# Optimization experiments

Hardware: AMD Instinct MI355X
Metric: run time of the kernel (lower is better)

Reference implementation:

```python
import jax, jax.numpy as jnp
import numpy as np

H = 256
NUM_REL = 480
NUM_ENT = 23000
N_TRIPLES = 8192
T = 10  # cur_ts == path_len window


def _lin_params(key, din, dout):
    kw, _ = jax.random.split(key)
    W = jax.random.normal(kw, (din, dout), dtype=jnp.float32) * 0.02
    b = jnp.zeros((dout,), dtype=jnp.float32)
    return W, b


def setup_inputs() -> dict:
    key = jax.random.key(0)
    ks = jax.random.split(key, 16)
    pre_emb = jax.random.normal(ks[0], (NUM_ENT, H), dtype=jnp.float32)
    r_emb = jax.random.normal(ks[1], (NUM_REL, H), dtype=jnp.float32)
    # history counts: sparse non-negative (zeros are masked to -1e9 in softmax)
    part = jax.random.uniform(ks[2], (N_TRIPLES, T * NUM_REL), dtype=jnp.float32)
    mask = jax.random.uniform(ks[3], (N_TRIPLES, T * NUM_REL)) < 0.3
    partial_embeding = jnp.where(mask, part, 0.0)
    sub_idx = jax.random.randint(ks[4], (N_TRIPLES,), 0, NUM_ENT)
    rel_idx = jax.random.randint(ks[5], (N_TRIPLES,), 0, NUM_REL)
    obj_idx = jax.random.randint(ks[6], (N_TRIPLES,), 0, NUM_ENT)
    Wm1, bm1 = _lin_params(ks[7], H, 2 * H)
    Wm2, bm2 = _lin_params(ks[8], 2 * H, H)
    Wattn, battn = _lin_params(ks[9], H, H)
    Wh1, bh1 = _lin_params(ks[10], H, H)
    Wh2, bh2 = _lin_params(ks[11], H, H)
    Walign, balign = _lin_params(ks[12], H, H)
    Wih = jax.random.normal(ks[13], (H, 3 * H), dtype=jnp.float32) * 0.02
    Whh = jax.random.normal(ks[14], (H, 3 * H), dtype=jnp.float32) * 0.02
    bih = jnp.zeros((3 * H,), dtype=jnp.float32)
    bhh = jnp.zeros((3 * H,), dtype=jnp.float32)
    return dict(pre_emb=pre_emb, r_emb=r_emb, partial_embeding=partial_embeding,
                sub_idx=sub_idx, rel_idx=rel_idx, obj_idx=obj_idx, cur_ts=T,
                Wm1=Wm1, bm1=bm1, Wm2=Wm2, bm2=bm2, Wattn=Wattn, battn=battn,
                Wh1=Wh1, bh1=bh1, Wh2=Wh2, bh2=bh2, Walign=Walign, balign=balign,
                Wih=Wih, Whh=Whh, bih=bih, bhh=bhh)


def _gru_cell(x, h, Wih, Whh, bih, bhh):
    # torch.nn.GRUCell math
    gi = x @ Wih + bih
    gh = h @ Whh + bhh
    i_r, i_z, i_n = jnp.split(gi, 3, axis=-1)
    h_r, h_z, h_n = jnp.split(gh, 3, axis=-1)
    r = jax.nn.sigmoid(i_r + h_r)
    z = jax.nn.sigmoid(i_z + h_z)
    n = jnp.tanh(i_n + r * h_n)
    return (1.0 - z) * n + z * h


def reference(pre_emb, r_emb, partial_embeding, sub_idx, rel_idx, obj_idx, cur_ts,
              Wm1, bm1, Wm2, bm2, Wattn, battn, Wh1, bh1, Wh2, bh2,
              Walign, balign, Wih, Whh, bih, bhh):
    n = partial_embeding.shape[0]
    num_rel = r_emb.shape[0]
    t = cur_ts  # path window covers [0, cur_ts)
    # relation mapping
    mapped_rel = (r_emb @ Wm1 + bm1) @ Wm2 + bm2            # [R, H]
    q_rel = mapped_rel[rel_idx]                               # [N, H]
    # attention logits base (loop-invariant): q W_attn mapped_rel^T
    base = (q_rel @ Wattn + battn) @ mapped_rel.T            # [N, R]
    # [N, t*R] -> [t, N, R] time-major slices
    hist = partial_embeding[:, : t * num_rel].reshape(n, t, num_rel).swapaxes(0, 1)
    h0 = jnp.zeros((n, mapped_rel.shape[1]), dtype=pre_emb.dtype)

    def step(h, cur):
        attn = cur * base
        attn = jax.nn.softmax(jnp.where(attn == 0, -1e9, attn), axis=1)
        x = attn @ mapped_rel                                 # [N, H]
        return _gru_cell(x, h, Wih, Whh, bih, bhh), None

    gru_hidden, _ = jax.lax.scan(step, h0, hist)
    # predicted history + match loss
    predicted_hist = 0.1 * ((q_rel @ Wh1 + bh1) @ Wh2 + bh2) + q_rel
    match_loss = jnp.mean((predicted_hist - gru_hidden) ** 2)
    # forward_forth (distmult)
    h2 = _gru_cell(q_rel, predicted_hist, Wih, Whh, bih, bhh)  # [N, H]
    sub = pre_emb[sub_idx]
    score_ = ((sub @ Walign + balign) * h2) @ (pre_emb @ Walign + balign).T  # [N, E]
    # BCE(sigmoid(score_), one_hot(obj)): per-elem -y*logsig(s) - (1-y)*logsig(-s)
    pos = score_[jnp.arange(n), obj_idx]
    path_loss = (-jnp.sum(jax.nn.log_sigmoid(-score_)) - jnp.sum(pos)) / (score_.size)
    score = jax.nn.sigmoid(score_)
    return match_loss, path_loss, score
```

## Files before the change

kernel.cpp:

```cpp
#include <hip/hip_runtime.h>
#include <hip/hip_bf16.h>
#include <stdint.h>

#define DEV __device__ __forceinline__

typedef unsigned short u16;
typedef __attribute__((ext_vector_type(8))) short bf16x8;
typedef __attribute__((ext_vector_type(4))) float f32x4;
typedef __attribute__((ext_vector_type(4))) unsigned short u16x4;

constexpr int H  = 256;
constexpr int R  = 480;
constexpr int NE = 23000;
constexpr int NT = 8192;
constexpr int TT = 10;

DEV u16 f2b(float f) {
  union { float f; unsigned u; } x; x.f = f;
  unsigned u = x.u;
  return (u16)((u + 0x7fffu + ((u >> 16) & 1u)) >> 16);
}
DEV float b2f(u16 h) {
  union { unsigned u; float f; } x; x.u = ((unsigned)h) << 16;
  return x.f;
}

DEV void gload_lds16(const u16* g, u16* lds) {
  __builtin_amdgcn_global_load_lds(
      (const __attribute__((address_space(1))) unsigned int*)g,
      (__attribute__((address_space(3))) unsigned int*)lds, 16, 0, 0);
}

__global__ void init_k(float* __restrict__ h, unsigned int* __restrict__ hb) {
  const int idx = blockIdx.x * 256 + threadIdx.x;
  h[idx] = 0.f;
  if (idx < (NT * H) / 2) hb[idx] = 0u;
}

__launch_bounds__(256)
__global__ void stageA_k(const float* __restrict__ r_emb,
                         const float* __restrict__ Wm1, const float* __restrict__ bm1,
                         const float* __restrict__ Wm2, const float* __restrict__ bm2,
                         const float* __restrict__ Wattn, const float* __restrict__ battn,
                         const float* __restrict__ Wih,
                         const float* __restrict__ Wh1, const float* __restrict__ bh1,
                         const float* __restrict__ Wh2, const float* __restrict__ bh2,
                         const float* __restrict__ Whh, const float* __restrict__ bhh,
                         const float* __restrict__ bih,
                         float* __restrict__ mapped, float* __restrict__ t1,
                         float* __restrict__ Pg, float* __restrict__ G2,
                         u16* __restrict__ MWT) {
  __shared__ float re[256], hid[512], mp[256], p1l[256], Pl[256];
  const int r = blockIdx.x, j = threadIdx.x;
  re[j] = r_emb[(size_t)r * 256 + j];
  __syncthreads();
  float s0 = bm1[j], s1 = bm1[j + 256];
  for (int k = 0; k < 256; ++k) {
    const float a = re[k];
    s0 += a * Wm1[(size_t)k * 512 + j];
    s1 += a * Wm1[(size_t)k * 512 + j + 256];
  }
  hid[j] = s0; hid[j + 256] = s1;
  __syncthreads();
  float m = bm2[j];
  for (int k = 0; k < 512; ++k) m += hid[k] * Wm2[(size_t)k * 256 + j];
  mp[j] = m; mapped[(size_t)r * 256 + j] = m;
  __syncthreads();
  float tv = battn[j];
  for (int k = 0; k < 256; ++k) tv += mp[k] * Wattn[(size_t)k * 256 + j];
  t1[(size_t)r * 256 + j] = tv;
  float mw0 = 0.f, mw1 = 0.f, mw2 = 0.f;
  for (int k = 0; k < 256; ++k) {
    const float a = mp[k];
    mw0 += a * Wih[(size_t)k * 768 + j];
    mw1 += a * Wih[(size_t)k * 768 + j + 256];
    mw2 += a * Wih[(size_t)k * 768 + j + 512];
  }
  MWT[(size_t)j * 480 + r] = f2b(mw0);
  MWT[(size_t)(j + 256) * 480 + r] = f2b(mw1);
  MWT[(size_t)(j + 512) * 480 + r] = f2b(mw2);
  float pv = bh1[j];
  for (int k = 0; k < 256; ++k) pv += mp[k] * Wh1[(size_t)k * 256 + j];
  p1l[j] = pv;
  __syncthreads();
  float Pv = bh2[j];
  for (int k = 0; k < 256; ++k) Pv += p1l[k] * Wh2[(size_t)k * 256 + j];
  Pv = 0.1f * Pv + mp[j];
  Pl[j] = Pv; Pg[(size_t)r * 256 + j] = Pv;
  __syncthreads();
  float pw0 = bhh[j], pw1 = bhh[j + 256], pw2 = bhh[j + 512];
  for (int k = 0; k < 256; ++k) {
    const float a = Pl[k];
    pw0 += a * Whh[(size_t)k * 768 + j];
    pw1 += a * Whh[(size_t)k * 768 + j + 256];
    pw2 += a * Whh[(size_t)k * 768 + j + 512];
  }
  const float rg = 1.f / (1.f + __expf(-(mw0 + bih[j] + pw0)));
  const float zg = 1.f / (1.f + __expf(-(mw1 + bih[j + 256] + pw1)));
  const float ng = tanhf(mw2 + bih[j + 512] + rg * pw2);
  G2[(size_t)r * 256 + j] = (1.f - zg) * ng + zg * Pv;
}

__global__ void sgemm_bt_k(const float* __restrict__ A, const float* __restrict__ W,
                           float* __restrict__ C, int M, int N, int K) {
  const int idx = blockIdx.x * 256 + threadIdx.x;
  if (idx >= M * N) return;
  const int i = idx / N, j = idx % N;
  float s = 0.f;
  const float* a = A + (size_t)i * K;
  const float* w = W + (size_t)j * K;
  for (int k = 0; k < K; ++k) s += a[k] * w[k];
  C[idx] = s;
}

__global__ void prep_k(const float* __restrict__ Whh, const float* __restrict__ Walign,
                       const float* __restrict__ bih, const float* __restrict__ bhh,
                       u16* __restrict__ WhhT, u16* __restrict__ WalignT,
                       float* __restrict__ bsum) {
  const int b = blockIdx.x, tid = threadIdx.x;
  if (b < 768) {
    WhhT[(size_t)b * 256 + tid] = f2b(Whh[(size_t)tid * 768 + b]);
  } else if (b < 1024) {
    const int n = b - 768;
    WalignT[(size_t)n * 256 + tid] = f2b(Walign[(size_t)tid * 256 + n]);
  } else {
    const int c = (b - 1024) * 256 + tid;
    if (c < 768) bsum[c] = bih[c] + (c < 512 ? bhh[c] : 0.f);
  }
}

__global__ void softmax_all_k(const float* __restrict__ part, const float* __restrict__ B480,
                              const int* __restrict__ rel_idx, u16* __restrict__ attn,
                              int t0) {
  const int task = blockIdx.x * 4 + (threadIdx.x >> 6);
  const int lane = threadIdx.x & 63;
  const int tt = task >> 13;
  const int i  = task & (NT - 1);
  const float* cur = part + (size_t)i * (TT * R) + (size_t)(t0 + tt) * R;
  const float* b = B480 + (size_t)rel_idx[i] * R;
  float v[8];
  float m = -3e38f;
  #pragma unroll
  for (int j = 0; j < 8; ++j) {
    const int r = lane + j * 64;
    float val = -1e9f;
    if (r < R) {
      const float c = cur[r];
      val = (c == 0.f) ? -1e9f : c * b[r];
      m = fmaxf(m, val);
    }
    v[j] = val;
  }
  #pragma unroll
  for (int o = 32; o; o >>= 1) m = fmaxf(m, __shfl_xor(m, o));
  float s = 0.f;
  #pragma unroll
  for (int j = 0; j < 8; ++j) {
    const int r = lane + j * 64;
    if (r < R) { v[j] = __expf(v[j] - m); s += v[j]; }
  }
  #pragma unroll
  for (int o = 32; o; o >>= 1) s += __shfl_xor(s, o);
  const float inv = 1.f / s;
  u16* arow = attn + (size_t)task * R;
  #pragma unroll
  for (int j = 0; j < 8; ++j) {
    const int r = lane + j * 64;
    if (r < R) arow[r] = f2b(v[j] * inv);
  }
}

__launch_bounds__(256)
__global__ void ghgates_k(const u16* __restrict__ hb, const u16* __restrict__ WhhT,
                          const float* __restrict__ bhh, const u16* __restrict__ gi,
                          float* __restrict__ h, u16* __restrict__ hb_out) {
  __shared__ __align__(16) u16 As[64 * 32];
  __shared__ __align__(16) u16 Bs[192 * 32];
  const int tid = threadIdx.x;
  const int lane = tid & 63;
  const int wv = tid >> 6;
  const int cg = blockIdx.x;
  const int m0 = blockIdx.y * 64;
  const int wr0 = wv * 16;
  const int fr = lane & 15;
  const int fq = lane >> 4;

  const int row_e = m0 + wr0 + fr;
  u16x4 g_r[4], g_z[4], g_n[4];
  f32x4 hv[4], bn;
  #pragma unroll
  for (int nc = 0; nc < 4; ++nc) {
    const int c = cg * 64 + nc * 16 + fq * 4;
    const size_t gb = (size_t)row_e * 768 + c;
    g_r[nc] = *(const u16x4*)&gi[gb];
    g_z[nc] = *(const u16x4*)&gi[gb + 256];
    g_n[nc] = *(const u16x4*)&gi[gb + 512];
    hv[nc] = *(const f32x4*)&h[(size_t)row_e * H + c];
  }
  {
    const int c = cg * 64 + fq * 4;
    bn = *(const f32x4*)&bhh[512 + c];
  }

  f32x4 acc[12] = {};
  for (int k0 = 0; k0 < H; k0 += 32) {
    __syncthreads();
    {
      const int row = tid >> 2, cc = tid & 3;
      gload_lds16(hb + (size_t)(m0 + row) * H + k0 + cc * 8,
                  &As[(wv * 64) * 8]);
    }
    #pragma unroll
    for (int it = 0; it < 3; ++it) {
      const int c = it * 256 + tid;
      const int vrow = c >> 2, cc = c & 3;
      const int col = (vrow >> 6) * 256 + cg * 64 + (vrow & 63);
      gload_lds16(WhhT + (size_t)col * H + k0 + cc * 8,
                  &Bs[(it * 256 + wv * 64) * 8]);
    }
    __syncthreads();
    const bf16x8 a = *(const bf16x8*)&As[(wr0 + fr) * 32 + fq * 8];
    bf16x8 b[12];
    #pragma unroll
    for (int ni = 0; ni < 12; ++ni)
      b[ni] = *(const bf16x8*)&Bs[(ni * 16 + fr) * 32 + fq * 8];
    #pragma unroll
    for (int ni = 0; ni < 12; ++ni)
      acc[ni] = __builtin_amdgcn_mfma_f32_16x16x32_bf16(b[ni], a, acc[ni], 0, 0, 0);
  }

  #pragma unroll
  for (int nc = 0; nc < 4; ++nc) {
    const int c = cg * 64 + nc * 16 + fq * 4;
    const f32x4 bnn = *(const f32x4*)&bhh[512 + c];
    const size_t hi = (size_t)row_e * H + c;
    f32x4 hn;
    u16x4 hb4;
    #pragma unroll
    for (int j = 0; j < 4; ++j) {
      const float rg = 1.f / (1.f + __expf(-(b2f(g_r[nc][j]) + acc[nc][j])));
      const float zg = 1.f / (1.f + __expf(-(b2f(g_z[nc][j]) + acc[4 + nc][j])));
      const float ng = tanhf(b2f(g_n[nc][j]) + rg * (acc[8 + nc][j] + bnn[j]));
      hn[j] = (1.f - zg) * ng + zg * hv[nc][j];
      hb4[j] = f2b(hn[j]);
    }
    *(f32x4*)&h[hi] = hn;
    *(u16x4*)&hb_out[hi] = hb4;
  }
}

__global__ void gather_sub_k(const float* __restrict__ pre, const int* __restrict__ sub,
                             u16* __restrict__ sb) {
  const int q = blockIdx.x * 256 + threadIdx.x;
  const int i = q >> 6, c = (q & 63) * 4;
  const f32x4 v = *(const f32x4*)&pre[(size_t)sub[i] * H + c];
  u16x4 o;
  #pragma unroll
  for (int j = 0; j < 4; ++j) o[j] = f2b(v[j]);
  *(u16x4*)&sb[(size_t)q * 4] = o;
}
__global__ void cvt_pre_k(const float* __restrict__ pre, u16* __restrict__ pb) {
  const int q = blockIdx.x * 256 + threadIdx.x;
  const f32x4 v = *(const f32x4*)&pre[(size_t)q * 4];
  u16x4 o;
  #pragma unroll
  for (int j = 0; j < 4; ++j) o[j] = f2b(v[j]);
  *(u16x4*)&pb[(size_t)q * 4] = o;
}

__global__ void pos_k(const u16* __restrict__ lhs, const u16* __restrict__ alT,
                      const int* __restrict__ obj, float* __restrict__ pos) {
  const int row = blockIdx.x * 4 + (threadIdx.x >> 6);
  const int lane = threadIdx.x & 63;
  const u16x4 av = *(const u16x4*)&lhs[(size_t)row * H + lane * 4];
  const u16x4 bv = *(const u16x4*)&alT[(size_t)obj[row] * H + lane * 4];
  float s = 0.f;
  #pragma unroll
  for (int j = 0; j < 4; ++j) s += b2f(av[j]) * b2f(bv[j]);
  #pragma unroll
  for (int o = 32; o; o >>= 1) s += __shfl_down(s, o);
  if (lane == 0) pos[row] = s;
}

__global__ void finalize_k(const float* __restrict__ mp, const float* __restrict__ sp,
                           const float* __restrict__ pos, float* __restrict__ out) {
  const int tid = threadIdx.x;
  float s1 = 0.f, s2 = 0.f, s3 = 0.f;
  for (int i = tid; i < 128; i += 256) s1 += mp[i];
  for (int i = tid; i < 11520; i += 256) s2 += sp[i];
  for (int i = tid; i < 8192; i += 256) s3 += pos[i];
  #pragma unroll
  for (int o = 32; o; o >>= 1) {
    s1 += __shfl_down(s1, o); s2 += __shfl_down(s2, o); s3 += __shfl_down(s3, o);
  }
  __shared__ float r1[4], r2[4], r3[4];
  if ((tid & 63) == 0) { r1[tid >> 6] = s1; r2[tid >> 6] = s2; r3[tid >> 6] = s3; }
  __syncthreads();
  if (tid == 0) {
    const float a = r1[0] + r1[1] + r1[2] + r1[3];
    const float b = r2[0] + r2[1] + r2[2] + r2[3];
    const float c = r3[0] + r3[1] + r3[2] + r3[3];
    out[0] = a / 2097152.f;
    out[1] = (b - c) / 188416000.f;
  }
}

template <int MODE>
__launch_bounds__(256)
__global__ void gemm_k(const u16* __restrict__ A, const u16* __restrict__ Bt,
                       const float* __restrict__ bias,
                       float* __restrict__ Cf, u16* __restrict__ Cb,
                       int M, int N, int K,
                       float* __restrict__ out2, float* __restrict__ part,
                       const int* __restrict__ rel_idx, const float* __restrict__ Pf,
                       const float* __restrict__ G2f, const float* __restrict__ hf) {
  __shared__ __align__(16) u16 As[128 * 32];
  __shared__ __align__(16) u16 Bs[128 * 32];
  __shared__ float red[4];
  const int tid = threadIdx.x;
  const int lane = tid & 63;
  const int wv = tid >> 6;
  const int nbx = gridDim.x;
  int flat = blockIdx.y * nbx + blockIdx.x;
  const int nwg = nbx * gridDim.y;
  if ((nwg & 7) == 0) flat = (flat & 7) * (nwg >> 3) + (flat >> 3);
  const int bx = flat % nbx;
  const int by = flat / nbx;
  const int m0 = by * 128;
  const int n0 = bx * 128;
  const int wm = (wv >> 1) * 64;
  const int wn = (wv & 1) * 64;
  const int fr = lane & 15;
  const int fq = lane >> 4;
  f32x4 acc[4][4] = {};

  for (int k0 = 0; k0 < K; k0 += 32) {
    __syncthreads();
    #pragma unroll
    for (int it = 0; it < 2; ++it) {
      const int c = it * 256 + tid;
      const int row = c >> 2;
      const int cc = c & 3;
      int gr = m0 + row; gr = gr < M ? gr : M - 1;
      gload_lds16(A + (size_t)gr * K + k0 + cc * 8, &As[(it * 256 + wv * 64) * 8]);
      int nr = n0 + row; nr = nr < N ? nr : N - 1;
      gload_lds16(Bt + (size_t)nr * K + k0 + cc * 8, &Bs[(it * 256 + wv * 64) * 8]);
    }
    __syncthreads();
    bf16x8 a[4], b[4];
    #pragma unroll
    for (int mi = 0; mi < 4; ++mi)
      a[mi] = *(const bf16x8*)&As[(wm + mi * 16 + fr) * 32 + fq * 8];
    #pragma unroll
    for (int ni = 0; ni < 4; ++ni)
      b[ni] = *(const bf16x8*)&Bs[(wn + ni * 16 + fr) * 32 + fq * 8];
    #pragma unroll
    for (int mi = 0; mi < 4; ++mi)
      #pragma unroll
      for (int ni = 0; ni < 4; ++ni)
        acc[mi][ni] = __builtin_amdgcn_mfma_f32_16x16x32_bf16(b[ni], a[mi], acc[mi][ni], 0, 0, 0);
  }

  float local = 0.f;
  #pragma unroll
  for (int mi = 0; mi < 4; ++mi) {
    const int rowm = m0 + wm + mi * 16 + fr;
    int rel = 0;
    if (MODE == 2) rel = rel_idx[rowm];
    #pragma unroll
    for (int ni = 0; ni < 4; ++ni) {
      const int col = n0 + wn + ni * 16 + fq * 4;
      if (rowm < M && col < N) {
        f32x4 v = acc[mi][ni];
        if (MODE == 0) {
          if (bias != nullptr) {
            const f32x4 bv = *(const f32x4*)&bias[col];
            #pragma unroll
            for (int j = 0; j < 4; ++j) v[j] += bv[j];
          }
          if (Cf) *(f32x4*)&Cf[(size_t)rowm * N + col] = v;
          if (Cb) {
            u16x4 o;
            #pragma unroll
            for (int j = 0; j < 4; ++j) o[j] = f2b(v[j]);
            *(u16x4*)&Cb[(size_t)rowm * N + col] = o;
          }
        } else if (MODE == 1) {
          f32x4 sg;
          #pragma unroll
          for (int j = 0; j < 4; ++j) {
            const float s = v[j];
            const float sig = 1.f / (1.f + __expf(-s));
            sg[j] = sig;
            const float om = 1.f - sig;
            local += (om > 0.f) ? -__logf(om) : s;
          }
          *(f32x4*)&out2[(size_t)rowm * N + col] = sg;
        } else {
          const f32x4 bv = *(const f32x4*)&bias[col];
          const f32x4 Pv = *(const f32x4*)&Pf[(size_t)rel * H + col];
          const f32x4 Gv = *(const f32x4*)&G2f[(size_t)rel * H + col];
          const f32x4 hv = *(const f32x4*)&hf[(size_t)rowm * H + col];
          u16x4 o;
          #pragma unroll
          for (int j = 0; j < 4; ++j) {
            const float d = Pv[j] - hv[j];
            local += d * d;
            o[j] = f2b((v[j] + bv[j]) * Gv[j]);
          }
          *(u16x4*)&Cb[(size_t)rowm * N + col] = o;
        }
      }
    }
  }
  if (MODE != 0) {
    #pragma unroll
    for (int o = 32; o; o >>= 1) local += __shfl_down(local, o);
    if (lane == 0) red[wv] = local;
    __syncthreads();
    if (tid == 0) part[blockIdx.y * gridDim.x + blockIdx.x] = red[0] + red[1] + red[2] + red[3];
  }
}

extern "C" void kernel_launch(void* const* d_in, const int* in_sizes, int n_in,
                              void* d_out, int out_size, void* d_ws, size_t ws_size,
                              hipStream_t stream) {
  const float* pre_emb = (const float*)d_in[0];
  const float* r_emb   = (const float*)d_in[1];
  const float* part_e  = (const float*)d_in[2];
  const int*   sub_idx = (const int*)d_in[3];
  const int*   rel_idx = (const int*)d_in[4];
  const int*   obj_idx = (const int*)d_in[5];
  const float* Wm1 = (const float*)d_in[7];  const float* bm1 = (const float*)d_in[8];
  const float* Wm2 = (const float*)d_in[9];  const float* bm2 = (const float*)d_in[10];
  const float* Wattn = (const float*)d_in[11]; const float* battn = (const float*)d_in[12];
  const float* Wh1 = (const float*)d_in[13]; const float* bh1 = (const float*)d_in[14];
  const float* Wh2 = (const float*)d_in[15]; const float* bh2 = (const float*)d_in[16];
  const float* Walign = (const float*)d_in[17]; const float* balign = (const float*)d_in[18];
  const float* Wih = (const float*)d_in[19]; const float* Whh = (const float*)d_in[20];
  const float* bih = (const float*)d_in[21]; const float* bhh = (const float*)d_in[22];
  float* out = (float*)d_out;

  char* w = (char*)d_ws;
  size_t off = 0;
  auto alloc = [&](size_t bytes) -> void* {
    off = (off + 255) & ~(size_t)255;
    void* p = w + off;
    off += bytes;
    return p;
  };
  float* mapped = (float*)alloc((size_t)R * H * 4);
  float* t1     = (float*)alloc((size_t)R * H * 4);
  float* B480   = (float*)alloc((size_t)R * R * 4);
  float* P      = (float*)alloc((size_t)R * H * 4);
  float* G2     = (float*)alloc((size_t)R * H * 4);
  u16* MWT      = (u16*)alloc((size_t)768 * R * 2);
  u16* WhhT     = (u16*)alloc((size_t)768 * H * 2);
  u16* WalignT  = (u16*)alloc((size_t)H * H * 2);
  float* bsum   = (float*)alloc(768 * 4);
  float* hbuf   = (float*)alloc((size_t)NT * H * 4);
  u16* hb0      = (u16*)alloc((size_t)NT * H * 2);
  u16* hb1      = (u16*)alloc((size_t)NT * H * 2);
  u16* lhs_b    = (u16*)alloc((size_t)NT * H * 2);
  u16* sub_b    = (u16*)alloc((size_t)NT * H * 2);
  u16* pre_b    = (u16*)alloc((size_t)NE * H * 2);
  u16* alT      = (u16*)alloc((size_t)NE * H * 2);
  float* mpart  = (float*)alloc(128 * 4);
  float* spart  = (float*)alloc(11520 * 4);
  float* posar  = (float*)alloc(8192 * 4);
  const size_t fixed_end = off;

  int chunkT = TT;
  u16 *attn_all = nullptr, *gi_all = nullptr;
  for (;;) {
    off = fixed_end;
    attn_all = (u16*)alloc((size_t)chunkT * NT * R * 2);
    gi_all   = (u16*)alloc((size_t)chunkT * NT * 768 * 2);
    if (off <= ws_size) break;
    if (chunkT == 1) return;
    chunkT = 1;
  }

  init_k<<<NT, 256, 0, stream>>>(hbuf, (unsigned int*)hb0);

  stageA_k<<<R, 256, 0, stream>>>(r_emb, Wm1, bm1, Wm2, bm2, Wattn, battn, Wih,
                                  Wh1, bh1, Wh2, bh2, Whh, bhh, bih,
                                  mapped, t1, P, G2, MWT);
  sgemm_bt_k<<<(R * R + 255) / 256, 256, 0, stream>>>(t1, mapped, B480, R, R, H);
  prep_k<<<1027, 256, 0, stream>>>(Whh, Walign, bih, bhh, WhhT, WalignT, bsum);

  u16* hcur = hb0;
  u16* hnxt = hb1;
  for (int t0 = 0; t0 < TT; t0 += chunkT) {
    softmax_all_k<<<chunkT * (NT / 4), 256, 0, stream>>>(part_e, B480, rel_idx, attn_all, t0);
    gemm_k<0><<<dim3(6, chunkT * (NT / 128)), 256, 0, stream>>>(
        attn_all, MWT, bsum, nullptr, gi_all, chunkT * NT, 768, R,
        nullptr, nullptr, nullptr, nullptr, nullptr, nullptr);
    for (int tt = 0; tt < chunkT; ++tt) {
      ghgates_k<<<dim3(4, NT / 64), 256, 0, stream>>>(
          hcur, WhhT, bhh, gi_all + (size_t)tt * NT * 768, hbuf, hnxt);
      u16* tmp = hcur; hcur = hnxt; hnxt = tmp;
    }
  }

  gather_sub_k<<<NT / 4, 256, 0, stream>>>(pre_emb, sub_idx, sub_b);
  gemm_k<2><<<dim3(2, 64), 256, 0, stream>>>(
      sub_b, WalignT, balign, nullptr, lhs_b, NT, H, H,
      nullptr, mpart, rel_idx, P, G2, hbuf);

  cvt_pre_k<<<NE / 4, 256, 0, stream>>>(pre_emb, pre_b);
  gemm_k<0><<<dim3(2, 180), 256, 0, stream>>>(
      pre_b, WalignT, balign, nullptr, alT, NE, H, H,
      nullptr, nullptr, nullptr, nullptr, nullptr, nullptr);

  gemm_k<1><<<dim3(180, 64), 256, 0, stream>>>(
      lhs_b, alT, nullptr, nullptr, nullptr, NT, NE, H,
      out + 2, spart, nullptr, nullptr, nullptr, nullptr);

  pos_k<<<2048, 256, 0, stream>>>(lhs_b, alT, obj_idx, posar);
  finalize_k<<<1, 256, 0, stream>>>(mpart, spart, posar, out);
}
```

Measured before the change: 1.134 ms.

## Fuse GRU time loop into one persistent scan kernel with LDS-resident hidden state

Replaces the ten per-timestep ghgates launches with a single scan kernel. Each block owns 32 rows and keeps the hidden state in registers, with a bf16 copy in swizzled LDS, across all timesteps, while double-buffering the Whh tiles. This removes the per-step launch overhead and the global round-trips of h. The generic GEMM moves to a K=64 step with an XOR-swizzled LDS layout, and the attention and MWT buffers are padded from 480 to 512 columns so K is aligned. The cost is only 256 blocks for the scan, which limits occupancy, plus Whh being re-streamed for every block and every step.

```diff
diff --git a/kernel.cpp b/kernel.cpp
--- a/kernel.cpp
+++ b/kernel.cpp
@@ -11,6 +11,7 @@
 
 constexpr int H  = 256;
 constexpr int R  = 480;
+constexpr int RP = 512;
 constexpr int NE = 23000;
 constexpr int NT = 8192;
 constexpr int TT = 10;
@@ -29,12 +30,6 @@
   __builtin_amdgcn_global_load_lds(
       (const __attribute__((address_space(1))) unsigned int*)g,
       (__attribute__((address_space(3))) unsigned int*)lds, 16, 0, 0);
-}
-
-__global__ void init_k(float* __restrict__ h, unsigned int* __restrict__ hb) {
-  const int idx = blockIdx.x * 256 + threadIdx.x;
-  h[idx] = 0.f;
-  if (idx < (NT * H) / 2) hb[idx] = 0u;
 }
 
 __launch_bounds__(256)
@@ -76,9 +71,9 @@
     mw1 += a * Wih[(size_t)k * 768 + j + 256];
     mw2 += a * Wih[(size_t)k * 768 + j + 512];
   }
-  MWT[(size_t)j * 480 + r] = f2b(mw0);
-  MWT[(size_t)(j + 256) * 480 + r] = f2b(mw1);
-  MWT[(size_t)(j + 512) * 480 + r] = f2b(mw2);
+  MWT[(size_t)j * RP + r] = f2b(mw0);
+  MWT[(size_t)(j + 256) * RP + r] = f2b(mw1);
+  MWT[(size_t)(j + 512) * RP + r] = f2b(mw2);
   float pv = bh1[j];
   for (int k = 0; k < 256; ++k) pv += mp[k] * Wh1[(size_t)k * 256 + j];
   p1l[j] = pv;
@@ -130,13 +125,12 @@
 }
 
 __global__ void softmax_all_k(const float* __restrict__ part, const float* __restrict__ B480,
-                              const int* __restrict__ rel_idx, u16* __restrict__ attn,
-                              int t0) {
+                              const int* __restrict__ rel_idx, u16* __restrict__ attn) {
   const int task = blockIdx.x * 4 + (threadIdx.x >> 6);
   const int lane = threadIdx.x & 63;
   const int tt = task >> 13;
   const int i  = task & (NT - 1);
-  const float* cur = part + (size_t)i * (TT * R) + (size_t)(t0 + tt) * R;
+  const float* cur = part + (size_t)i * (TT * R) + (size_t)tt * R;
   const float* b = B480 + (size_t)rel_idx[i] * R;
   float v[8];
   float m = -3e38f;
@@ -162,90 +156,124 @@
   #pragma unroll
   for (int o = 32; o; o >>= 1) s += __shfl_xor(s, o);
   const float inv = 1.f / s;
-  u16* arow = attn + (size_t)task * R;
+  u16* arow = attn + (size_t)task * RP;
   #pragma unroll
   for (int j = 0; j < 8; ++j) {
     const int r = lane + j * 64;
-    if (r < R) arow[r] = f2b(v[j] * inv);
+    arow[r] = (r < R) ? f2b(v[j] * inv) : (u16)0;
   }
 }
 
 __launch_bounds__(256)
-__global__ void ghgates_k(const u16* __restrict__ hb, const u16* __restrict__ WhhT,
-                          const float* __restrict__ bhh, const u16* __restrict__ gi,
-                          float* __restrict__ h, u16* __restrict__ hb_out) {
-  __shared__ __align__(16) u16 As[64 * 32];
-  __shared__ __align__(16) u16 Bs[192 * 32];
+__global__ void scan_k(const u16* __restrict__ WhhT, const float* __restrict__ bhh,
+                       const u16* __restrict__ gi_all, float* __restrict__ hbuf) {
+  __shared__ __align__(16) u16 As[32 * 256];
+  __shared__ __align__(16) u16 Bs[2][192 * 64];
   const int tid = threadIdx.x;
   const int lane = tid & 63;
   const int wv = tid >> 6;
-  const int cg = blockIdx.x;
-  const int m0 = blockIdx.y * 64;
-  const int wr0 = wv * 16;
+  const int rf = wv >> 1;
+  const int ch = wv & 1;
   const int fr = lane & 15;
   const int fq = lane >> 4;
-
-  const int row_e = m0 + wr0 + fr;
-  u16x4 g_r[4], g_z[4], g_n[4];
-  f32x4 hv[4], bn;
-  #pragma unroll
-  for (int nc = 0; nc < 4; ++nc) {
-    const int c = cg * 64 + nc * 16 + fq * 4;
-    const size_t gb = (size_t)row_e * 768 + c;
-    g_r[nc] = *(const u16x4*)&gi[gb];
-    g_z[nc] = *(const u16x4*)&gi[gb + 256];
-    g_n[nc] = *(const u16x4*)&gi[gb + 512];
-    hv[nc] = *(const f32x4*)&h[(size_t)row_e * H + c];
-  }
-  {
-    const int c = cg * 64 + fq * 4;
-    bn = *(const f32x4*)&bhh[512 + c];
-  }
-
-  f32x4 acc[12] = {};
-  for (int k0 = 0; k0 < H; k0 += 32) {
+  const int row_l = rf * 16 + fr;
+  const int grow = blockIdx.x * 32 + row_l;
+  const int sw = (fr & 7) * 8;
+
+  auto stageB = [&](int buf, int cg, int k0) {
+    #pragma unroll
+    for (int it = 0; it < 6; ++it) {
+      const int c = it * 256 + tid;
+      const int vr = c >> 3, s = c & 7;
+      const int vcol = ((vr >> 6) * 256) + cg * 64 + (vr & 63);
+      gload_lds16(WhhT + (size_t)vcol * 256 + k0 + ((s ^ (vr & 7)) * 8),
+                  &Bs[buf][(it * 256 + wv * 64) * 8]);
+    }
+  };
+
+  float hreg[4][2][4];
+  #pragma unroll
+  for (int cg = 0; cg < 4; ++cg)
+    #pragma unroll
+    for (int nn = 0; nn < 2; ++nn)
+      #pragma unroll
+      for (int j = 0; j < 4; ++j) hreg[cg][nn][j] = 0.f;
+
+  for (int t = 0; t < TT; ++t) {
+    const u16* gi = gi_all + (size_t)t * NT * 768;
+    #pragma unroll
+    for (int cg = 0; cg < 4; ++cg) {
+      f32x4 acc[6] = {};
+      u16x4 gv[3][2];
+      #pragma unroll
+      for (int nn = 0; nn < 2; ++nn) {
+        const int c = cg * 64 + ch * 32 + nn * 16 + fq * 4;
+        const size_t gb = (size_t)grow * 768 + c;
+        gv[0][nn] = *(const u16x4*)&gi[gb];
+        gv[1][nn] = *(const u16x4*)&gi[gb + 256];
+        gv[2][nn] = *(const u16x4*)&gi[gb + 512];
+      }
+      if (t > 0) {
+        stageB(0, cg, 0);
+        #pragma unroll
+        for (int ki = 0; ki < 4; ++ki) {
+          const int cb = ki & 1;
+          if (ki < 3) {
+            stageB(cb ^ 1, cg, (ki + 1) * 64);
+            asm volatile("s_waitcnt vmcnt(6)" ::: "memory");
+          } else {
+            asm volatile("s_waitcnt vmcnt(0)" ::: "memory");
+          }
+          __builtin_amdgcn_sched_barrier(0);
+          __builtin_amdgcn_s_barrier();
+          #pragma unroll
+          for (int kk = 0; kk < 2; ++kk) {
+            const int ko = (ki * 64 + kk * 32 + fq * 8) ^ sw;
+            const bf16x8 a = *(const bf16x8*)&As[row_l * 256 + ko];
+            const int bo = (kk * 32 + fq * 8) ^ sw;
+            #pragma unroll
+            for (int g = 0; g < 3; ++g)
+              #pragma unroll
+              for (int nn = 0; nn < 2; ++nn) {
+                const int vr = g * 64 + ch * 32 + nn * 16 + fr;
+                const bf16x8 b = *(const bf16x8*)&Bs[cb][vr * 64 + bo];
+                acc[g * 2 + nn] =
+                    __builtin_amdgcn_mfma_f32_16x16x32_bf16(b, a, acc[g * 2 + nn], 0, 0, 0);
+              }
+          }
+          __builtin_amdgcn_s_barrier();
+        }
+      }
+      #pragma unroll
+      for (int nn = 0; nn < 2; ++nn) {
+        const int c = cg * 64 + ch * 32 + nn * 16 + fq * 4;
+        const f32x4 bn = *(const f32x4*)&bhh[512 + c];
+        #pragma unroll
+        for (int j = 0; j < 4; ++j) {
+          const float rg = 1.f / (1.f + __expf(-(b2f(gv[0][nn][j]) + acc[nn][j])));
+          const float zg = 1.f / (1.f + __expf(-(b2f(gv[1][nn][j]) + acc[2 + nn][j])));
+          const float ng = tanhf(b2f(gv[2][nn][j]) + rg * (acc[4 + nn][j] + bn[j]));
+          hreg[cg][nn][j] = (1.f - zg) * ng + zg * hreg[cg][nn][j];
+        }
+      }
+    }
+    #pragma unroll
+    for (int cg = 0; cg < 4; ++cg)
+      #pragma unroll
+      for (int nn = 0; nn < 2; ++nn) {
+        const int c = cg * 64 + ch * 32 + nn * 16 + fq * 4;
+        u16x4 o;
+        #pragma unroll
+        for (int j = 0; j < 4; ++j) o[j] = f2b(hreg[cg][nn][j]);
+        *(u16x4*)&As[row_l * 256 + (c ^ sw)] = o;
+        if (t == TT - 1) {
+          f32x4 hv;
+          #pragma unroll
+          for (int j = 0; j < 4; ++j) hv[j] = hreg[cg][nn][j];
+          *(f32x4*)&hbuf[(size_t)grow * 256 + c] = hv;
+        }
+      }
     __syncthreads();
-    {
-      const int row = tid >> 2, cc = tid & 3;
-      gload_lds16(hb + (size_t)(m0 + row) * H + k0 + cc * 8,
-                  &As[(wv * 64) * 8]);
-    }
-    #pragma unroll
-    for (int it = 0; it < 3; ++it) {
-      const int c = it * 256 + tid;
-      const int vrow = c >> 2, cc = c & 3;
-      const int col = (vrow >> 6) * 256 + cg * 64 + (vrow & 63);
-      gload_lds16(WhhT + (size_t)col * H + k0 + cc * 8,
-                  &Bs[(it * 256 + wv * 64) * 8]);
-    }
-    __syncthreads();
-    const bf16x8 a = *(const bf16x8*)&As[(wr0 + fr) * 32 + fq * 8];
-    bf16x8 b[12];
-    #pragma unroll
-    for (int ni = 0; ni < 12; ++ni)
-      b[ni] = *(const bf16x8*)&Bs[(ni * 16 + fr) * 32 + fq * 8];
-    #pragma unroll
-    for (int ni = 0; ni < 12; ++ni)
-      acc[ni] = __builtin_amdgcn_mfma_f32_16x16x32_bf16(b[ni], a, acc[ni], 0, 0, 0);
-  }
-
-  #pragma unroll
-  for (int nc = 0; nc < 4; ++nc) {
-    const int c = cg * 64 + nc * 16 + fq * 4;
-    const f32x4 bnn = *(const f32x4*)&bhh[512 + c];
-    const size_t hi = (size_t)row_e * H + c;
-    f32x4 hn;
-    u16x4 hb4;
-    #pragma unroll
-    for (int j = 0; j < 4; ++j) {
-      const float rg = 1.f / (1.f + __expf(-(b2f(g_r[nc][j]) + acc[nc][j])));
-      const float zg = 1.f / (1.f + __expf(-(b2f(g_z[nc][j]) + acc[4 + nc][j])));
-      const float ng = tanhf(b2f(g_n[nc][j]) + rg * (acc[8 + nc][j] + bnn[j]));
-      hn[j] = (1.f - zg) * ng + zg * hv[nc][j];
-      hb4[j] = f2b(hn[j]);
-    }
-    *(f32x4*)&h[hi] = hn;
-    *(u16x4*)&hb_out[hi] = hb4;
   }
 }
 
@@ -314,8 +342,8 @@
                        float* __restrict__ out2, float* __restrict__ part,
                        const int* __restrict__ rel_idx, const float* __restrict__ Pf,
                        const float* __restrict__ G2f, const float* __restrict__ hf) {
-  __shared__ __align__(16) u16 As[128 * 32];
-  __shared__ __align__(16) u16 Bs[128 * 32];
+  __shared__ __align__(16) u16 As[128 * 64];
+  __shared__ __align__(16) u16 Bs[128 * 64];
   __shared__ float red[4];
   const int tid = threadIdx.x;
   const int lane = tid & 63;
@@ -332,33 +360,38 @@
   const int wn = (wv & 1) * 64;
   const int fr = lane & 15;
   const int fq = lane >> 4;
+  const int sw = (lane & 7) * 8;
   f32x4 acc[4][4] = {};
 
-  for (int k0 = 0; k0 < K; k0 += 32) {
+  for (int k0 = 0; k0 < K; k0 += 64) {
     __syncthreads();
     #pragma unroll
-    for (int it = 0; it < 2; ++it) {
+    for (int it = 0; it < 4; ++it) {
       const int c = it * 256 + tid;
-      const int row = c >> 2;
-      const int cc = c & 3;
+      const int row = c >> 3, s = c & 7;
+      const int sc = (s ^ (row & 7)) * 8;
       int gr = m0 + row; gr = gr < M ? gr : M - 1;
-      gload_lds16(A + (size_t)gr * K + k0 + cc * 8, &As[(it * 256 + wv * 64) * 8]);
+      gload_lds16(A + (size_t)gr * K + k0 + sc, &As[(it * 256 + wv * 64) * 8]);
       int nr = n0 + row; nr = nr < N ? nr : N - 1;
-      gload_lds16(Bt + (size_t)nr * K + k0 + cc * 8, &Bs[(it * 256 + wv * 64) * 8]);
+      gload_lds16(Bt + (size_t)nr * K + k0 + sc, &Bs[(it * 256 + wv * 64) * 8]);
     }
     __syncthreads();
-    bf16x8 a[4], b[4];
-    #pragma unroll
-    for (int mi = 0; mi < 4; ++mi)
-      a[mi] = *(const bf16x8*)&As[(wm + mi * 16 + fr) * 32 + fq * 8];
-    #pragma unroll
-    for (int ni = 0; ni < 4; ++ni)
-      b[ni] = *(const bf16x8*)&Bs[(wn + ni * 16 + fr) * 32 + fq * 8];
-    #pragma unroll
-    for (int mi = 0; mi < 4; ++mi)
+    #pragma unroll
+    for (int kk = 0; kk < 2; ++kk) {
+      const int ko = (kk * 32 + fq * 8) ^ sw;
+      bf16x8 a[4], b[4];
+      #pragma unroll
+      for (int mi = 0; mi < 4; ++mi)
+        a[mi] = *(const bf16x8*)&As[(wm + mi * 16 + fr) * 64 + ko];
       #pragma unroll
       for (int ni = 0; ni < 4; ++ni)
-        acc[mi][ni] = __builtin_amdgcn_mfma_f32_16x16x32_bf16(b[ni], a[mi], acc[mi][ni], 0, 0, 0);
+        b[ni] = *(const bf16x8*)&Bs[(wn + ni * 16 + fr) * 64 + ko];
+      #pragma unroll
+      for (int mi = 0; mi < 4; ++mi)
+        #pragma unroll
+        for (int ni = 0; ni < 4; ++ni)
+          acc[mi][ni] = __builtin_amdgcn_mfma_f32_16x16x32_bf16(b[ni], a[mi], acc[mi][ni], 0, 0, 0);
+    }
   }
 
   float local = 0.f;
@@ -454,13 +487,11 @@
   float* B480   = (float*)alloc((size_t)R * R * 4);
   float* P      = (float*)alloc((size_t)R * H * 4);
   float* G2     = (float*)alloc((size_t)R * H * 4);
-  u16* MWT      = (u16*)alloc((size_t)768 * R * 2);
+  u16* MWT      = (u16*)alloc((size_t)768 * RP * 2);
   u16* WhhT     = (u16*)alloc((size_t)768 * H * 2);
   u16* WalignT  = (u16*)alloc((size_t)H * H * 2);
   float* bsum   = (float*)alloc(768 * 4);
   float* hbuf   = (float*)alloc((size_t)NT * H * 4);
-  u16* hb0      = (u16*)alloc((size_t)NT * H * 2);
-  u16* hb1      = (u16*)alloc((size_t)NT * H * 2);
   u16* lhs_b    = (u16*)alloc((size_t)NT * H * 2);
   u16* sub_b    = (u16*)alloc((size_t)NT * H * 2);
   u16* pre_b    = (u16*)alloc((size_t)NE * H * 2);
@@ -468,40 +499,22 @@
   float* mpart  = (float*)alloc(128 * 4);
   float* spart  = (float*)alloc(11520 * 4);
   float* posar  = (float*)alloc(8192 * 4);
-  const size_t fixed_end = off;
-
-  int chunkT = TT;
-  u16 *attn_all = nullptr, *gi_all = nullptr;
-  for (;;) {
-    off = fixed_end;
-    attn_all = (u16*)alloc((size_t)chunkT * NT * R * 2);
-    gi_all   = (u16*)alloc((size_t)chunkT * NT * 768 * 2);
-    if (off <= ws_size) break;
-    if (chunkT == 1) return;
-    chunkT = 1;
-  }
-
-  init_k<<<NT, 256, 0, stream>>>(hbuf, (unsigned int*)hb0);
-
+  u16* attn_all = (u16*)alloc((size_t)TT * NT * RP * 2);
+  u16* gi_all   = (u16*)alloc((size_t)TT * NT * 768 * 2);
+  if (off > ws_size) return;
+
+  hipMemsetAsync(MWT, 0, (size_t)768 * RP * 2, stream);
   stageA_k<<<R, 256, 0, stream>>>(r_emb, Wm1, bm1, Wm2, bm2, Wattn, battn, Wih,
                                   Wh1, bh1, Wh2, bh2, Whh, bhh, bih,
                                   mapped, t1, P, G2, MWT);
   sgemm_bt_k<<<(R * R + 255) / 256, 256, 0, stream>>>(t1, mapped, B480, R, R, H);
   prep_k<<<1027, 256, 0, stream>>>(Whh, Walign, bih, bhh, WhhT, WalignT, bsum);
 
-  u16* hcur = hb0;
-  u16* hnxt = hb1;
-  for (int t0 = 0; t0 < TT; t0 += chunkT) {
-    softmax_all_k<<<chunkT * (NT / 4), 256, 0, stream>>>(part_e, B480, rel_idx, attn_all, t0);
-    gemm_k<0><<<dim3(6, chunkT * (NT / 128)), 256, 0, stream>>>(
-        attn_all, MWT, bsum, nullptr, gi_all, chunkT * NT, 768, R,
-        nullptr, nullptr, nullptr, nullptr, nullptr, nullptr);
-    for (int tt = 0; tt < chunkT; ++tt) {
-      ghgates_k<<<dim3(4, NT / 64), 256, 0, stream>>>(
-          hcur, WhhT, bhh, gi_all + (size_t)tt * NT * 768, hbuf, hnxt);
-      u16* tmp = hcur; hcur = hnxt; hnxt = tmp;
-    }
-  }
+  softmax_all_k<<<TT * (NT / 4), 256, 0, stream>>>(part_e, B480, rel_idx, attn_all);
+  gemm_k<0><<<dim3(6, TT * (NT / 128)), 256, 0, stream>>>(
+      attn_all, MWT, bsum, nullptr, gi_all, TT * NT, 768, RP,
+      nullptr, nullptr, nullptr, nullptr, nullptr, nullptr);
+  scan_k<<<NT / 32, 256, 0, stream>>>(WhhT, bhh, gi_all, hbuf);
 
   gather_sub_k<<<NT / 4, 256, 0, stream>>>(pre_emb, sub_idx, sub_b);
   gemm_k<2><<<dim3(2, 64), 256, 0, stream>>>(
```

Result: faster. 1.109 ms (-2.2%).
